# Kernel tuning notes

Measured on AMD Instinct MI355X. Metric: run time of the kernel, lower is better.

The kernel has to match this reference:

```python
import jax, jax.numpy as jnp
import numpy as np

TAU = 20.0            # membrane time constant
TAU_ADAPT = 20.0      # threshold adaptation time constant
BETA = 1.8            # adaptation strength (n_regular=0 -> all neurons adaptive)
DAMPENING = 1.0       # surrogate-gradient dampening
REF_PERIOD = 2.0      # refractory period (steps)
THR = 0.03            # base threshold
INTERNAL_CURRENT = 0.0


@jax.custom_vjp
def spike_fn(v_sc):
    # Heaviside forward; triangular pseudo-derivative backward.
    return (v_sc > 0.0).astype(v_sc.dtype)

def _spike_fwd(v_sc):
    return spike_fn(v_sc), v_sc

def _spike_bwd(v_sc, g):
    # triangular pseudo-derivative: dampening * max(0, 1 - |v_sc|) (sharpness=1)
    return (g * DAMPENING * jnp.maximum(0.0, 1.0 - jnp.abs(v_sc)),)

spike_fn.defvjp(_spike_fwd, _spike_bwd)


def setup_inputs() -> dict:
    key = jax.random.key(0)
    kx, kin, krec = jax.random.split(key, 3)
    B, T, NI, N = 128, 500, 256, 256
    x = jax.random.normal(kx, (B, T, NI), dtype=jnp.float32)
    w_in = jax.random.normal(kin, (NI, N), dtype=jnp.float32) / np.float32(np.sqrt(NI))
    w_rec = jax.random.normal(krec, (N, N), dtype=jnp.float32) / np.float32(np.sqrt(N))
    zeros = jnp.zeros((B, N), dtype=jnp.float32)
    return {"x": x, "w_in": w_in, "w_rec": w_rec,
            "z0": zeros, "v0": zeros, "a0": zeros, "lsd0": zeros}


def _lsnn_scan(x, w_in, w_rec, z0, v0, a0, lsd0):
    n = w_rec.shape[0]
    mask = 1.0 - jnp.eye(n, dtype=x.dtype)          # zero out self-connections
    w_rec_m = mask * w_rec
    decay_v = jnp.exp(jnp.asarray(-1.0 / TAU, x.dtype))
    decay_a = jnp.exp(jnp.asarray(-1.0 / TAU_ADAPT, x.dtype))
    beta_vec = jnp.full((n,), BETA, dtype=x.dtype)  # n_regular = 0

    def step(carry, x_t):
        old_z, old_v, old_a, lsd = carry
        # currents: external + masked recurrent + constant internal
        i_in = x_t @ w_in + old_z @ w_rec_m + INTERNAL_CURRENT
        # adaptive threshold dynamics
        new_a = decay_a * old_a + (1.0 - decay_a) * old_z
        thr = THR + new_a * beta_vec
        # voltage dynamics with reset current
        i_reset = -thr * old_z
        new_v = decay_v * old_v + (1.0 - decay_v) * i_in + i_reset
        # surrogate spike
        v_sc = (new_v - thr) / thr
        z = spike_fn(v_sc)
        # refractoriness
        non_ref = (lsd >= REF_PERIOD).astype(x.dtype)
        z = non_ref * z
        new_lsd = (lsd + 1.0) * (1.0 - z)
        return (z, new_v, new_a, new_lsd), (z, new_v, thr, v_sc)

    x_t_first = jnp.swapaxes(x, 0, 1)               # [T, B, n_in]
    _, (zs, vs, thrs, vscs) = jax.lax.scan(step, (z0, v0, a0, lsd0), x_t_first)
    # stack the 4 per-step outputs -> [4, T, B, N]
    return jnp.stack([zs, vs, thrs, vscs], axis=0)


def reference(x, w_in, w_rec, z0, v0, a0, lsd0):
    return _lsnn_scan(x, w_in, w_rec, z0, v0, a0, lsd0)
```

## Files before the change

kernel.cpp:

```cpp
#include <hip/hip_runtime.h>

#define T_STEPS 500
#define N_NEUR  256
#define N_IN    256
#define N_BATCH 128

__global__ __launch_bounds__(256) void xw_gemm_kernel(
    const float* __restrict__ A,
    const float* __restrict__ W,
    float* __restrict__ C)
{
    __shared__ float As[16][129];
    __shared__ float Bs[16][68];
    const int tid = threadIdx.x;
    const int bm  = blockIdx.x;
    const int bn  = blockIdx.y;
    const int ty  = tid >> 4;
    const int tx  = tid & 15;
    const int arow  = tid >> 1;
    const int akoff = (tid & 1) * 8;
    const int brow  = tid >> 4;
    const int bcol  = (tid & 15) * 4;
    const float* Ab = A + (size_t)bm * 128 * 256;

    float acc[8][4];
#pragma unroll
    for (int i = 0; i < 8; ++i)
#pragma unroll
        for (int j = 0; j < 4; ++j) acc[i][j] = 0.f;

    for (int k0 = 0; k0 < 256; k0 += 16) {
        float4 av0 = *(const float4*)(Ab + (size_t)arow * 256 + k0 + akoff);
        float4 av1 = *(const float4*)(Ab + (size_t)arow * 256 + k0 + akoff + 4);
        float4 bv  = *(const float4*)(W + (size_t)(k0 + brow) * 256 + bn * 64 + bcol);
        __syncthreads();
        As[akoff + 0][arow] = av0.x; As[akoff + 1][arow] = av0.y;
        As[akoff + 2][arow] = av0.z; As[akoff + 3][arow] = av0.w;
        As[akoff + 4][arow] = av1.x; As[akoff + 5][arow] = av1.y;
        As[akoff + 6][arow] = av1.z; As[akoff + 7][arow] = av1.w;
        *(float4*)&Bs[brow][bcol] = bv;
        __syncthreads();
#pragma unroll
        for (int kk = 0; kk < 16; ++kk) {
            float a[8], b[4];
#pragma unroll
            for (int i = 0; i < 8; ++i) a[i] = As[kk][ty * 8 + i];
#pragma unroll
            for (int j = 0; j < 4; ++j) b[j] = Bs[kk][tx * 4 + j];
#pragma unroll
            for (int i = 0; i < 8; ++i)
#pragma unroll
                for (int j = 0; j < 4; ++j)
                    acc[i][j] += a[i] * b[j];
        }
    }
    const int crow = bm * 128 + ty * 8;
    const int ccol = bn * 64 + tx * 4;
#pragma unroll
    for (int i = 0; i < 8; ++i) {
        float4 v = make_float4(acc[i][0], acc[i][1], acc[i][2], acc[i][3]);
        *(float4*)(C + (size_t)(crow + i) * 256 + ccol) = v;
    }
}

__global__ void prep_wrec_kernel(const float* __restrict__ w_rec,
                                 float* __restrict__ wz)
{
    int i = blockIdx.x * 256 + threadIdx.x;
    if (i < 256 * 256) {
        int r = i >> 8, c = i & 255;
        wz[i] = (r == c) ? 0.f : w_rec[i];
    } else {
        wz[i] = 0.f;
    }
}

__device__ __forceinline__ unsigned long long rfl64(unsigned long long q) {
    unsigned hi = (unsigned)__builtin_amdgcn_readfirstlane((int)(q >> 32));
    unsigned lo = (unsigned)__builtin_amdgcn_readfirstlane((int)(unsigned)q);
    return ((unsigned long long)hi << 32) | (unsigned long long)lo;
}

__global__ __launch_bounds__(256) void lsnn_scan2_kernel(
    const float* __restrict__ xw,
    const float* __restrict__ wz,
    const float* __restrict__ z0, const float* __restrict__ v0,
    const float* __restrict__ a0, const float* __restrict__ lsd0,
    float* __restrict__ out)
{
    const int b    = blockIdx.x;
    const int n    = threadIdx.x;
    const int lane = n & 63;
    const int wid  = n >> 6;

    __shared__ unsigned long long msk[2][4];

    const float dv   = (float)0.9512294245007140018;
    const float omdv = 1.0f - dv;

    const int bn = b * N_NEUR + n;
    float z   = z0[bn];
    float v   = v0[bn];
    float a   = a0[bn];
    float lsd = lsd0[bn];

    {
        unsigned long long wm = __ballot(z != 0.f);
        if (lane == 0) msk[0][wid] = wm;
    }
    __syncthreads();

    float x_next = xw[((size_t)b * T_STEPS) * N_NEUR + n];
    const size_t PL = (size_t)T_STEPS * N_BATCH * N_NEUR;

    for (int t = 0; t < T_STEPS; ++t) {
        float x_cur = x_next;
        {
            int tn = (t + 1 < T_STEPS) ? t + 1 : t;
            x_next = xw[((size_t)b * T_STEPS + tn) * N_NEUR + n];
        }

        const int rb = t & 1;
        unsigned long long m0 = rfl64(msk[rb][0]);
        unsigned long long m1 = rfl64(msk[rb][1]);
        unsigned long long m2 = rfl64(msk[rb][2]);
        unsigned long long m3 = rfl64(msk[rb][3]);

        const int c0 = __popcll(m0), c1 = __popcll(m1);
        const int c2 = __popcll(m2), c3 = __popcll(m3);
        const int mx = max(max(c0, c1), max(c2, c3));

        float p0 = 0.f, p1 = 0.f, p2 = 0.f, p3 = 0.f;
        for (int i0 = 0; i0 < mx; i0 += 8) {
            int id0[8], id1[8], id2[8], id3[8];
#pragma unroll
            for (int j = 0; j < 8; ++j) {
                id0[j] = m0 ? (__builtin_ctzll(m0) + 0)   : 256;  m0 &= m0 - 1;
                id1[j] = m1 ? (__builtin_ctzll(m1) + 64)  : 256;  m1 &= m1 - 1;
                id2[j] = m2 ? (__builtin_ctzll(m2) + 128) : 256;  m2 &= m2 - 1;
                id3[j] = m3 ? (__builtin_ctzll(m3) + 192) : 256;  m3 &= m3 - 1;
            }
            float w0[8], w1[8], w2[8], w3[8];
#pragma unroll
            for (int j = 0; j < 8; ++j) {
                w0[j] = wz[id0[j] * N_NEUR + n];
                w1[j] = wz[id1[j] * N_NEUR + n];
                w2[j] = wz[id2[j] * N_NEUR + n];
                w3[j] = wz[id3[j] * N_NEUR + n];
            }
#pragma unroll
            for (int j = 0; j < 8; ++j) {
                p0 += w0[j]; p1 += w1[j]; p2 += w2[j]; p3 += w3[j];
            }
        }
        float i_rec = ((p0 + p1) + p2) + p3;

        float i_in  = x_cur + i_rec;
        float new_a = dv * a + omdv * z;
        float thr   = 0.03f + new_a * 1.8f;
        float new_v = dv * v + omdv * i_in - thr * z;
        float v_sc  = (new_v - thr) / thr;
        float zs    = (v_sc > 0.f) ? 1.f : 0.f;
        zs          = (lsd >= 2.0f) ? zs : 0.f;
        float new_lsd = (lsd + 1.f) * (1.f - zs);

        size_t o = (size_t)t * (N_BATCH * N_NEUR) + (size_t)b * N_NEUR + n;
        __builtin_nontemporal_store(zs,    out + o);
        __builtin_nontemporal_store(new_v, out + o + PL);
        __builtin_nontemporal_store(thr,   out + o + 2 * PL);
        __builtin_nontemporal_store(v_sc,  out + o + 3 * PL);

        v = new_v; a = new_a; lsd = new_lsd; z = zs;

        {
            unsigned long long wm = __ballot(zs != 0.f);
            if (lane == 0) msk[rb ^ 1][wid] = wm;
        }
        __syncthreads();
    }
}

template <bool USE_XW>
__global__ __launch_bounds__(256) void lsnn_scan_kernel(
    const float* __restrict__ xin,
    const float* __restrict__ w_in,
    const float* __restrict__ w_rec,
    const float* __restrict__ z0, const float* __restrict__ v0,
    const float* __restrict__ a0, const float* __restrict__ lsd0,
    float* __restrict__ out)
{
    const int b    = blockIdx.x;
    const int n    = threadIdx.x;
    const int lane = n & 63;
    const int wid  = n >> 6;

    __shared__ int   cnt4[4];
    __shared__ int   act[256];
    __shared__ float xsh[256];

    const float dv   = (float)0.9512294245007140018;
    const float omdv = 1.0f - dv;

    const int base_bn = b * N_NEUR + n;
    float z   = z0[base_bn];
    float v   = v0[base_bn];
    float a   = a0[base_bn];
    float lsd = lsd0[base_bn];

    act[n] = 0;
    {
        unsigned long long wm = __ballot(z != 0.f);
        if (lane == 0) cnt4[wid] = __popcll(wm);
        if (z != 0.f) {
            int pos = __popcll(wm & ((1ull << lane) - 1ull));
            act[wid * 64 + pos] = n;
        }
        if (!USE_XW) xsh[n] = xin[((size_t)b * T_STEPS) * N_IN + n];
    }
    __syncthreads();

    float x_next = USE_XW ? xin[((size_t)b * T_STEPS) * N_NEUR + n] : 0.f;

    for (int t = 0; t < T_STEPS; ++t) {
        float x_cur = x_next;
        if (USE_XW) {
            int tn = (t + 1 < T_STEPS) ? t + 1 : t;
            x_next = xin[((size_t)b * T_STEPS + tn) * N_NEUR + n];
        }
        const int cs0 = cnt4[0], cs1 = cnt4[1], cs2 = cnt4[2], cs3 = cnt4[3];
        int mx = max(max(cs0, cs1), max(cs2, cs3));
        float r0 = 0.f, r1 = 0.f, r2 = 0.f, r3 = 0.f;
        for (int i0 = 0; i0 < mx; i0 += 8) {
            float wv[4][8];
            bool  ok[4][8];
#pragma unroll
            for (int s = 0; s < 4; ++s) {
                const int cs = (s == 0) ? cs0 : (s == 1) ? cs1 : (s == 2) ? cs2 : cs3;
#pragma unroll
                for (int j = 0; j < 8; ++j) {
                    int ii = i0 + j;
                    int m  = act[s * 64 + (ii < cs ? ii : 0)] & 255;
                    wv[s][j] = w_rec[m * N_NEUR + n];
                    ok[s][j] = (ii < cs) && (m != n);
                }
            }
#pragma unroll
            for (int j = 0; j < 8; ++j) r0 += ok[0][j] ? wv[0][j] : 0.f;
#pragma unroll
            for (int j = 0; j < 8; ++j) r1 += ok[1][j] ? wv[1][j] : 0.f;
#pragma unroll
            for (int j = 0; j < 8; ++j) r2 += ok[2][j] ? wv[2][j] : 0.f;
#pragma unroll
            for (int j = 0; j < 8; ++j) r3 += ok[3][j] ? wv[3][j] : 0.f;
        }
        float i_rec = ((r0 + r1) + r2) + r3;

        float xdot;
        if (USE_XW) {
            xdot = x_cur;
        } else {
            float s = 0.f;
#pragma unroll 8
            for (int m = 0; m < N_IN; ++m) s += xsh[m] * w_in[m * N_NEUR + n];
            xdot = s;
        }
        float i_in = xdot + i_rec;

        float new_a = dv * a + omdv * z;
        float thr   = 0.03f + new_a * 1.8f;
        float new_v = dv * v + omdv * i_in - thr * z;
        float v_sc  = (new_v - thr) / thr;
        float zs    = (v_sc > 0.f) ? 1.f : 0.f;
        zs          = (lsd >= 2.0f) ? zs : 0.f;
        float new_lsd = (lsd + 1.f) * (1.f - zs);

        const size_t PL = (size_t)T_STEPS * N_BATCH * N_NEUR;
        size_t o = (size_t)t * (N_BATCH * N_NEUR) + (size_t)b * N_NEUR + n;
        out[o]          = zs;
        out[o + PL]     = new_v;
        out[o + 2 * PL] = thr;
        out[o + 3 * PL] = v_sc;

        v = new_v; a = new_a; lsd = new_lsd; z = zs;

        __syncthreads();
        unsigned long long wm = __ballot(zs != 0.f);
        if (lane == 0) cnt4[wid] = __popcll(wm);
        if (zs != 0.f) {
            int pos = __popcll(wm & ((1ull << lane) - 1ull));
            act[wid * 64 + pos] = n;
        }
        if (!USE_XW && (t + 1 < T_STEPS))
            xsh[n] = xin[((size_t)b * T_STEPS + t + 1) * N_IN + n];
        __syncthreads();
    }
}

extern "C" void kernel_launch(void* const* d_in, const int* in_sizes, int n_in,
                              void* d_out, int out_size, void* d_ws, size_t ws_size,
                              hipStream_t stream) {
    const float* x     = (const float*)d_in[0];
    const float* w_in  = (const float*)d_in[1];
    const float* w_rec = (const float*)d_in[2];
    const float* z0    = (const float*)d_in[3];
    const float* v0    = (const float*)d_in[4];
    const float* a0    = (const float*)d_in[5];
    const float* lsd0  = (const float*)d_in[6];
    float* out = (float*)d_out;

    const size_t xw_bytes = (size_t)N_BATCH * T_STEPS * N_NEUR * sizeof(float);
    const size_t wz_bytes = (size_t)257 * 256 * sizeof(float);

    if (ws_size >= xw_bytes + wz_bytes) {
        float* xw = (float*)d_ws;
        float* wz = (float*)((char*)d_ws + xw_bytes);
        prep_wrec_kernel<<<257, 256, 0, stream>>>(w_rec, wz);
        dim3 grid(500, 4, 1);
        xw_gemm_kernel<<<grid, 256, 0, stream>>>(x, w_in, xw);
        lsnn_scan2_kernel<<<N_BATCH, 256, 0, stream>>>(
            xw, wz, z0, v0, a0, lsd0, out);
    } else if (ws_size >= xw_bytes) {
        float* xw = (float*)d_ws;
        dim3 grid(500, 4, 1);
        xw_gemm_kernel<<<grid, 256, 0, stream>>>(x, w_in, xw);
        lsnn_scan_kernel<true><<<N_BATCH, 256, 0, stream>>>(
            xw, nullptr, w_rec, z0, v0, a0, lsd0, out);
    } else {
        lsnn_scan_kernel<false><<<N_BATCH, 256, 0, stream>>>(
            x, w_in, w_rec, z0, v0, a0, lsd0, out);
    }
}
```

Before: 897.8 us.

## Keep recurrent weights in registers with 4-way split dense dot per neuron

Replaces the sparse spike-index gather of recurrent weights from global memory with a dense 256-term dot product. Each neuron is split across 4 threads, each holding 64 weights in registers, with spikes shared through LDS and partial sums combined by DPP lane broadcasts. Block size grows to 1024 threads, and the four output planes are written one per thread segment. This removes per-step global gathers and mask decoding, but does a fixed amount of FMA work per step regardless of sparsity, and 64 weights per thread at 1024 threads puts pressure on the register file.

```diff
diff --git a/kernel.cpp b/kernel.cpp
--- a/kernel.cpp
+++ b/kernel.cpp
@@ -75,28 +75,29 @@
     }
 }
 
-__device__ __forceinline__ unsigned long long rfl64(unsigned long long q) {
-    unsigned hi = (unsigned)__builtin_amdgcn_readfirstlane((int)(q >> 32));
-    unsigned lo = (unsigned)__builtin_amdgcn_readfirstlane((int)(unsigned)q);
-    return ((unsigned long long)hi << 32) | (unsigned long long)lo;
-}
-
-__global__ __launch_bounds__(256) void lsnn_scan2_kernel(
+__global__ __launch_bounds__(1024) void lsnn_scan3_kernel(
     const float* __restrict__ xw,
     const float* __restrict__ wz,
     const float* __restrict__ z0, const float* __restrict__ v0,
     const float* __restrict__ a0, const float* __restrict__ lsd0,
     float* __restrict__ out)
 {
-    const int b    = blockIdx.x;
-    const int n    = threadIdx.x;
-    const int lane = n & 63;
-    const int wid  = n >> 6;
-
-    __shared__ unsigned long long msk[2][4];
+    const int b   = blockIdx.x;
+    const int t0  = threadIdx.x;
+    const int n   = t0 >> 2;
+    const int seg = t0 & 3;
+
+    __shared__ __align__(16) float zsh[2][4][72];
 
     const float dv   = (float)0.9512294245007140018;
     const float omdv = 1.0f - dv;
+
+    float w[64];
+    {
+        const float* wc = wz + (size_t)seg * 64 * N_NEUR + n;
+#pragma unroll
+        for (int k = 0; k < 64; ++k) w[k] = wc[(size_t)k * N_NEUR];
+    }
 
     const int bn = b * N_NEUR + n;
     float z   = z0[bn];
@@ -104,10 +105,7 @@
     float a   = a0[bn];
     float lsd = lsd0[bn];
 
-    {
-        unsigned long long wm = __ballot(z != 0.f);
-        if (lane == 0) msk[0][wid] = wm;
-    }
+    if (seg == 0) zsh[0][n >> 6][n & 63] = z;
     __syncthreads();
 
     float x_next = xw[((size_t)b * T_STEPS) * N_NEUR + n];
@@ -119,41 +117,25 @@
             int tn = (t + 1 < T_STEPS) ? t + 1 : t;
             x_next = xw[((size_t)b * T_STEPS + tn) * N_NEUR + n];
         }
-
         const int rb = t & 1;
-        unsigned long long m0 = rfl64(msk[rb][0]);
-        unsigned long long m1 = rfl64(msk[rb][1]);
-        unsigned long long m2 = rfl64(msk[rb][2]);
-        unsigned long long m3 = rfl64(msk[rb][3]);
-
-        const int c0 = __popcll(m0), c1 = __popcll(m1);
-        const int c2 = __popcll(m2), c3 = __popcll(m3);
-        const int mx = max(max(c0, c1), max(c2, c3));
-
-        float p0 = 0.f, p1 = 0.f, p2 = 0.f, p3 = 0.f;
-        for (int i0 = 0; i0 < mx; i0 += 8) {
-            int id0[8], id1[8], id2[8], id3[8];
-#pragma unroll
-            for (int j = 0; j < 8; ++j) {
-                id0[j] = m0 ? (__builtin_ctzll(m0) + 0)   : 256;  m0 &= m0 - 1;
-                id1[j] = m1 ? (__builtin_ctzll(m1) + 64)  : 256;  m1 &= m1 - 1;
-                id2[j] = m2 ? (__builtin_ctzll(m2) + 128) : 256;  m2 &= m2 - 1;
-                id3[j] = m3 ? (__builtin_ctzll(m3) + 192) : 256;  m3 &= m3 - 1;
-            }
-            float w0[8], w1[8], w2[8], w3[8];
-#pragma unroll
-            for (int j = 0; j < 8; ++j) {
-                w0[j] = wz[id0[j] * N_NEUR + n];
-                w1[j] = wz[id1[j] * N_NEUR + n];
-                w2[j] = wz[id2[j] * N_NEUR + n];
-                w3[j] = wz[id3[j] * N_NEUR + n];
-            }
-#pragma unroll
-            for (int j = 0; j < 8; ++j) {
-                p0 += w0[j]; p1 += w1[j]; p2 += w2[j]; p3 += w3[j];
-            }
-        }
-        float i_rec = ((p0 + p1) + p2) + p3;
+
+        const float* zr = &zsh[rb][seg][0];
+        float p = 0.f;
+#pragma unroll
+        for (int k4 = 0; k4 < 16; ++k4) {
+            float4 zv = *(const float4*)(zr + 4 * k4);
+            p = fmaf(zv.x, w[4 * k4 + 0], p);
+            p = fmaf(zv.y, w[4 * k4 + 1], p);
+            p = fmaf(zv.z, w[4 * k4 + 2], p);
+            p = fmaf(zv.w, w[4 * k4 + 3], p);
+        }
+
+        const int pi = __float_as_int(p);
+        const float q0 = __int_as_float(__builtin_amdgcn_mov_dpp(pi, 0x00, 0xF, 0xF, true));
+        const float q1 = __int_as_float(__builtin_amdgcn_mov_dpp(pi, 0x55, 0xF, 0xF, true));
+        const float q2 = __int_as_float(__builtin_amdgcn_mov_dpp(pi, 0xAA, 0xF, 0xF, true));
+        const float q3 = __int_as_float(__builtin_amdgcn_mov_dpp(pi, 0xFF, 0xF, 0xF, true));
+        float i_rec = ((q0 + q1) + q2) + q3;
 
         float i_in  = x_cur + i_rec;
         float new_a = dv * a + omdv * z;
@@ -165,17 +147,13 @@
         float new_lsd = (lsd + 1.f) * (1.f - zs);
 
         size_t o = (size_t)t * (N_BATCH * N_NEUR) + (size_t)b * N_NEUR + n;
-        __builtin_nontemporal_store(zs,    out + o);
-        __builtin_nontemporal_store(new_v, out + o + PL);
-        __builtin_nontemporal_store(thr,   out + o + 2 * PL);
-        __builtin_nontemporal_store(v_sc,  out + o + 3 * PL);
+        float outv = (seg == 0) ? zs : (seg == 1) ? new_v
+                   : (seg == 2) ? thr : v_sc;
+        __builtin_nontemporal_store(outv, out + o + (size_t)seg * PL);
 
         v = new_v; a = new_a; lsd = new_lsd; z = zs;
 
-        {
-            unsigned long long wm = __ballot(zs != 0.f);
-            if (lane == 0) msk[rb ^ 1][wid] = wm;
-        }
+        if (seg == 0) zsh[rb ^ 1][n >> 6][n & 63] = zs;
         __syncthreads();
     }
 }
@@ -317,7 +295,7 @@
         prep_wrec_kernel<<<257, 256, 0, stream>>>(w_rec, wz);
         dim3 grid(500, 4, 1);
         xw_gemm_kernel<<<grid, 256, 0, stream>>>(x, w_in, xw);
-        lsnn_scan2_kernel<<<N_BATCH, 256, 0, stream>>>(
+        lsnn_scan3_kernel<<<N_BATCH, 1024, 0, stream>>>(
             xw, wz, z0, v0, a0, lsd0, out);
     } else if (ws_size >= xw_bytes) {
         float* xw = (float*)d_ws;
```

Result: faster. 748.8 us (-16.6%).

## Split recurrent sparse sum across four waves per neuron and widen GEMM tile

Applied to the files above, without the earlier changes.

The scan kernel now runs 1024 threads per batch, with four waves per neuron group. Each wave handles one 64-neuron source segment of the spike mask, so the serial gather loop covers one segment instead of the longest of four. Partial sums are reduced through shared memory, and each wave stores one of the four output planes. This adds an extra barrier per step and redundant state updates in exchange for a shorter per-step critical path. The input GEMM also uses 128x128 tiles with 8x8 per-thread outputs to raise arithmetic intensity.

```diff
diff --git a/kernel.cpp b/kernel.cpp
--- a/kernel.cpp
+++ b/kernel.cpp
@@ -5,13 +5,13 @@
 #define N_IN    256
 #define N_BATCH 128
 
-__global__ __launch_bounds__(256) void xw_gemm_kernel(
+__global__ __launch_bounds__(256) void xw_gemm2_kernel(
     const float* __restrict__ A,
     const float* __restrict__ W,
     float* __restrict__ C)
 {
-    __shared__ float As[16][129];
-    __shared__ float Bs[16][68];
+    __shared__ float As[16][132];
+    __shared__ float Bs[16][132];
     const int tid = threadIdx.x;
     const int bm  = blockIdx.x;
     const int bn  = blockIdx.y;
@@ -20,46 +20,50 @@
     const int arow  = tid >> 1;
     const int akoff = (tid & 1) * 8;
     const int brow  = tid >> 4;
-    const int bcol  = (tid & 15) * 4;
+    const int bcol  = (tid & 15) * 8;
     const float* Ab = A + (size_t)bm * 128 * 256;
 
-    float acc[8][4];
+    float acc[8][8];
 #pragma unroll
     for (int i = 0; i < 8; ++i)
 #pragma unroll
-        for (int j = 0; j < 4; ++j) acc[i][j] = 0.f;
+        for (int j = 0; j < 8; ++j) acc[i][j] = 0.f;
 
     for (int k0 = 0; k0 < 256; k0 += 16) {
         float4 av0 = *(const float4*)(Ab + (size_t)arow * 256 + k0 + akoff);
         float4 av1 = *(const float4*)(Ab + (size_t)arow * 256 + k0 + akoff + 4);
-        float4 bv  = *(const float4*)(W + (size_t)(k0 + brow) * 256 + bn * 64 + bcol);
+        float4 bv0 = *(const float4*)(W + (size_t)(k0 + brow) * 256 + bn * 128 + bcol);
+        float4 bv1 = *(const float4*)(W + (size_t)(k0 + brow) * 256 + bn * 128 + bcol + 4);
         __syncthreads();
         As[akoff + 0][arow] = av0.x; As[akoff + 1][arow] = av0.y;
         As[akoff + 2][arow] = av0.z; As[akoff + 3][arow] = av0.w;
         As[akoff + 4][arow] = av1.x; As[akoff + 5][arow] = av1.y;
         As[akoff + 6][arow] = av1.z; As[akoff + 7][arow] = av1.w;
-        *(float4*)&Bs[brow][bcol] = bv;
+        *(float4*)&Bs[brow][bcol]     = bv0;
+        *(float4*)&Bs[brow][bcol + 4] = bv1;
         __syncthreads();
 #pragma unroll
         for (int kk = 0; kk < 16; ++kk) {
-            float a[8], b[4];
+            float a[8], b[8];
 #pragma unroll
             for (int i = 0; i < 8; ++i) a[i] = As[kk][ty * 8 + i];
 #pragma unroll
-            for (int j = 0; j < 4; ++j) b[j] = Bs[kk][tx * 4 + j];
+            for (int j = 0; j < 8; ++j) b[j] = Bs[kk][tx * 8 + j];
 #pragma unroll
             for (int i = 0; i < 8; ++i)
 #pragma unroll
-                for (int j = 0; j < 4; ++j)
+                for (int j = 0; j < 8; ++j)
                     acc[i][j] += a[i] * b[j];
         }
     }
     const int crow = bm * 128 + ty * 8;
-    const int ccol = bn * 64 + tx * 4;
+    const int ccol = bn * 128 + tx * 8;
 #pragma unroll
     for (int i = 0; i < 8; ++i) {
-        float4 v = make_float4(acc[i][0], acc[i][1], acc[i][2], acc[i][3]);
-        *(float4*)(C + (size_t)(crow + i) * 256 + ccol) = v;
+        float4 v0 = make_float4(acc[i][0], acc[i][1], acc[i][2], acc[i][3]);
+        float4 v1 = make_float4(acc[i][4], acc[i][5], acc[i][6], acc[i][7]);
+        *(float4*)(C + (size_t)(crow + i) * 256 + ccol)     = v0;
+        *(float4*)(C + (size_t)(crow + i) * 256 + ccol + 4) = v1;
     }
 }
 
@@ -81,19 +85,23 @@
     return ((unsigned long long)hi << 32) | (unsigned long long)lo;
 }
 
-__global__ __launch_bounds__(256) void lsnn_scan2_kernel(
+__global__ __launch_bounds__(1024) void lsnn_scan4_kernel(
     const float* __restrict__ xw,
     const float* __restrict__ wz,
     const float* __restrict__ z0, const float* __restrict__ v0,
     const float* __restrict__ a0, const float* __restrict__ lsd0,
     float* __restrict__ out)
 {
+    const int tid  = threadIdx.x;
     const int b    = blockIdx.x;
-    const int n    = threadIdx.x;
-    const int lane = n & 63;
-    const int wid  = n >> 6;
+    const int w    = tid >> 6;
+    const int lane = tid & 63;
+    const int s    = w & 3;
+    const int g    = w >> 2;
+    const int n    = g * 64 + lane;
 
     __shared__ unsigned long long msk[2][4];
+    __shared__ float pl[16][72];
 
     const float dv   = (float)0.9512294245007140018;
     const float omdv = 1.0f - dv;
@@ -106,7 +114,7 @@
 
     {
         unsigned long long wm = __ballot(z != 0.f);
-        if (lane == 0) msk[0][wid] = wm;
+        if (s == 0 && lane == 0) msk[0][g] = wm;
     }
     __syncthreads();
 
@@ -119,41 +127,33 @@
             int tn = (t + 1 < T_STEPS) ? t + 1 : t;
             x_next = xw[((size_t)b * T_STEPS + tn) * N_NEUR + n];
         }
-
         const int rb = t & 1;
-        unsigned long long m0 = rfl64(msk[rb][0]);
-        unsigned long long m1 = rfl64(msk[rb][1]);
-        unsigned long long m2 = rfl64(msk[rb][2]);
-        unsigned long long m3 = rfl64(msk[rb][3]);
-
-        const int c0 = __popcll(m0), c1 = __popcll(m1);
-        const int c2 = __popcll(m2), c3 = __popcll(m3);
-        const int mx = max(max(c0, c1), max(c2, c3));
-
-        float p0 = 0.f, p1 = 0.f, p2 = 0.f, p3 = 0.f;
-        for (int i0 = 0; i0 < mx; i0 += 8) {
-            int id0[8], id1[8], id2[8], id3[8];
+
+        unsigned long long m = rfl64(msk[rb][s]);
+        const int cnt = __popcll(m);
+
+        float p = 0.f;
+        for (int i0 = 0; i0 < cnt; i0 += 8) {
+            int ro[8];
 #pragma unroll
             for (int j = 0; j < 8; ++j) {
-                id0[j] = m0 ? (__builtin_ctzll(m0) + 0)   : 256;  m0 &= m0 - 1;
-                id1[j] = m1 ? (__builtin_ctzll(m1) + 64)  : 256;  m1 &= m1 - 1;
-                id2[j] = m2 ? (__builtin_ctzll(m2) + 128) : 256;  m2 &= m2 - 1;
-                id3[j] = m3 ? (__builtin_ctzll(m3) + 192) : 256;  m3 &= m3 - 1;
+                ro[j] = (m ? (s * 64 + __builtin_ctzll(m)) : 256) * N_NEUR;
+                m &= m - 1;
             }
-            float w0[8], w1[8], w2[8], w3[8];
-#pragma unroll
-            for (int j = 0; j < 8; ++j) {
-                w0[j] = wz[id0[j] * N_NEUR + n];
-                w1[j] = wz[id1[j] * N_NEUR + n];
-                w2[j] = wz[id2[j] * N_NEUR + n];
-                w3[j] = wz[id3[j] * N_NEUR + n];
-            }
-#pragma unroll
-            for (int j = 0; j < 8; ++j) {
-                p0 += w0[j]; p1 += w1[j]; p2 += w2[j]; p3 += w3[j];
-            }
-        }
-        float i_rec = ((p0 + p1) + p2) + p3;
+            float wv[8];
+#pragma unroll
+            for (int j = 0; j < 8; ++j) wv[j] = wz[ro[j] + n];
+#pragma unroll
+            for (int j = 0; j < 8; ++j) p += wv[j];
+        }
+
+        pl[w][lane] = p;
+        __syncthreads();
+        float q0 = pl[g * 4 + 0][lane];
+        float q1 = pl[g * 4 + 1][lane];
+        float q2 = pl[g * 4 + 2][lane];
+        float q3 = pl[g * 4 + 3][lane];
+        float i_rec = ((q0 + q1) + q2) + q3;
 
         float i_in  = x_cur + i_rec;
         float new_a = dv * a + omdv * z;
@@ -165,16 +165,15 @@
         float new_lsd = (lsd + 1.f) * (1.f - zs);
 
         size_t o = (size_t)t * (N_BATCH * N_NEUR) + (size_t)b * N_NEUR + n;
-        __builtin_nontemporal_store(zs,    out + o);
-        __builtin_nontemporal_store(new_v, out + o + PL);
-        __builtin_nontemporal_store(thr,   out + o + 2 * PL);
-        __builtin_nontemporal_store(v_sc,  out + o + 3 * PL);
+        float outv = (s == 0) ? zs : (s == 1) ? new_v
+                   : (s == 2) ? thr : v_sc;
+        __builtin_nontemporal_store(outv, out + o + (size_t)s * PL);
 
         v = new_v; a = new_a; lsd = new_lsd; z = zs;
 
         {
             unsigned long long wm = __ballot(zs != 0.f);
-            if (lane == 0) msk[rb ^ 1][wid] = wm;
+            if (s == 0 && lane == 0) msk[rb ^ 1][g] = wm;
         }
         __syncthreads();
     }
@@ -234,14 +233,14 @@
             float wv[4][8];
             bool  ok[4][8];
 #pragma unroll
-            for (int s = 0; s < 4; ++s) {
-                const int cs = (s == 0) ? cs0 : (s == 1) ? cs1 : (s == 2) ? cs2 : cs3;
+            for (int sgi = 0; sgi < 4; ++sgi) {
+                const int cs = (sgi == 0) ? cs0 : (sgi == 1) ? cs1 : (sgi == 2) ? cs2 : cs3;
 #pragma unroll
                 for (int j = 0; j < 8; ++j) {
                     int ii = i0 + j;
-                    int m  = act[s * 64 + (ii < cs ? ii : 0)] & 255;
-                    wv[s][j] = w_rec[m * N_NEUR + n];
-                    ok[s][j] = (ii < cs) && (m != n);
+                    int m  = act[sgi * 64 + (ii < cs ? ii : 0)] & 255;
+                    wv[sgi][j] = w_rec[m * N_NEUR + n];
+                    ok[sgi][j] = (ii < cs) && (m != n);
                 }
             }
 #pragma unroll
@@ -259,10 +258,10 @@
         if (USE_XW) {
             xdot = x_cur;
         } else {
-            float s = 0.f;
+            float sum = 0.f;
 #pragma unroll 8
-            for (int m = 0; m < N_IN; ++m) s += xsh[m] * w_in[m * N_NEUR + n];
-            xdot = s;
+            for (int m = 0; m < N_IN; ++m) sum += xsh[m] * w_in[m * N_NEUR + n];
+            xdot = sum;
         }
         float i_in = xdot + i_rec;
 
@@ -315,14 +314,14 @@
         float* xw = (float*)d_ws;
         float* wz = (float*)((char*)d_ws + xw_bytes);
         prep_wrec_kernel<<<257, 256, 0, stream>>>(w_rec, wz);
-        dim3 grid(500, 4, 1);
-        xw_gemm_kernel<<<grid, 256, 0, stream>>>(x, w_in, xw);
-        lsnn_scan2_kernel<<<N_BATCH, 256, 0, stream>>>(
+        dim3 grid(500, 2, 1);
+        xw_gemm2_kernel<<<grid, 256, 0, stream>>>(x, w_in, xw);
+        lsnn_scan4_kernel<<<N_BATCH, 1024, 0, stream>>>(
             xw, wz, z0, v0, a0, lsd0, out);
     } else if (ws_size >= xw_bytes) {
         float* xw = (float*)d_ws;
-        dim3 grid(500, 4, 1);
-        xw_gemm_kernel<<<grid, 256, 0, stream>>>(x, w_in, xw);
+        dim3 grid(500, 2, 1);
+        xw_gemm2_kernel<<<grid, 256, 0, stream>>>(x, w_in, xw);
         lsnn_scan_kernel<true><<<N_BATCH, 256, 0, stream>>>(
             xw, nullptr, w_rec, z0, v0, a0, lsd0, out);
     } else {
```

New measurement: 810.8 us. 9.7% less time.
